# Kernel tuning notes

Measured on AMD Instinct MI355X. Metric: run time of the kernel, lower is better.

Reference implementation:

```python
import jax, jax.numpy as jnp
import numpy as np

N, F, E, C = 50000, 128, 800000, 10

def setup_inputs() -> dict:
    key = jax.random.key(0)
    ks = jax.random.split(key, 16)
    s = 1.0 / np.sqrt(F)
    def u(k, shape):
        return jax.random.uniform(k, shape, jnp.float32, -s, s)
    inp = {
        "x": jax.random.normal(ks[0], (N, F), jnp.float32),
        "edge_index": jax.random.randint(ks[1], (2, E), 0, N),
    }
    for i, p in enumerate(["1", "2"]):
        b = 2 + i * 5
        inp["W" + p] = u(ks[b], (F, F))          # EvolveGCNO initial_weight
        inp["wih" + p] = u(ks[b + 1], (3 * F, F))  # GRU input weights (r,z,n)
        inp["whh" + p] = u(ks[b + 2], (3 * F, F))  # GRU hidden weights
        inp["bih" + p] = u(ks[b + 3], (3 * F,))
        inp["bhh" + p] = u(ks[b + 4], (3 * F,))
    inp["lin_w"] = u(ks[12], (C, F))
    inp["lin_b"] = u(ks[13], (C,))
    return inp

def gru_step(x, h, wih, whh, bih, bhh):
    # torch.nn.GRU single step; gate order r, z, n
    gi = x @ wih.T + bih
    gh = h @ whh.T + bhh
    ir, iz, inn = jnp.split(gi, 3, axis=-1)
    hr, hz, hn = jnp.split(gh, 3, axis=-1)
    r = jax.nn.sigmoid(ir + hr)
    z = jax.nn.sigmoid(iz + hz)
    n = jnp.tanh(inn + r * hn)
    return (1.0 - z) * n + z * h

def gcn_conv(W, x, src, dst):
    # GCNConv_Fixed_W: gcn_norm with self-loops, then aggregate (x @ W)
    n = x.shape[0]
    loop = jnp.arange(n)
    s = jnp.concatenate([src, loop])
    d = jnp.concatenate([dst, loop])
    deg = jax.ops.segment_sum(jnp.ones(s.shape[0], x.dtype), d, num_segments=n)
    dinv = jnp.where(deg > 0, jax.lax.rsqrt(deg), 0.0)
    norm = dinv[s] * dinv[d]                 # [E+N]
    xw = x @ W                               # [N, F]
    return jax.ops.segment_sum(norm[:, None] * xw[s], d, num_segments=n)

def evolve_gcno(x, src, dst, W0, wih, whh, bih, bhh):
    # weight evolved by GRU with input = hidden = current weight
    W = gru_step(W0, W0, wih, whh, bih, bhh)
    return gcn_conv(W, x, src, dst)

def reference(x, edge_index, W1, wih1, whh1, bih1, bhh1,
              W2, wih2, whh2, bih2, bhh2, lin_w, lin_b):
    src, dst = edge_index[0], edge_index[1]
    h = jax.nn.relu(evolve_gcno(x, src, dst, W1, wih1, whh1, bih1, bhh1))
    # dropout is identity in eval mode
    h = jax.nn.relu(evolve_gcno(h, src, dst, W2, wih2, whh2, bih2, bhh2))
    logits = h @ lin_w.T + lin_b
    return jax.nn.log_softmax(logits, axis=1)
```

## Files before the change

kernel.cpp:

```cpp
#include <hip/hip_runtime.h>
#include <cstddef>
#include <cstdint>

#define F 128
#define C_OUT 10
#define SB 256

typedef short bf16x8 __attribute__((ext_vector_type(8)));
typedef float f32x4  __attribute__((ext_vector_type(4)));
typedef float f32x2  __attribute__((ext_vector_type(2)));

__device__ __forceinline__ unsigned short bf16_rne(float f) {
  unsigned u = __float_as_uint(f);
  return (unsigned short)((u + 0x7FFFu + ((u >> 16) & 1u)) >> 16);
}

__global__ void gru_evolve2_k(const float* __restrict__ W01, const float* __restrict__ wih1,
                              const float* __restrict__ whh1, const float* __restrict__ bih1,
                              const float* __restrict__ bhh1,
                              const float* __restrict__ W02, const float* __restrict__ wih2,
                              const float* __restrict__ whh2, const float* __restrict__ bih2,
                              const float* __restrict__ bhh2,
                              unsigned short* __restrict__ Bhi1, unsigned short* __restrict__ Bhi2,
                              int* __restrict__ counts, int n) {
  if ((int)blockIdx.x >= 128) {
    int i = ((int)blockIdx.x - 128) * SB + threadIdx.x;
    if (i < n) counts[i] = 0;
    return;
  }
  int t = blockIdx.x * 256 + threadIdx.x;
  int layer = t >> 14;
  int tt = t & 16383;
  const float* W0  = layer ? W02  : W01;
  const float* wih = layer ? wih2 : wih1;
  const float* whh = layer ? whh2 : whh1;
  const float* bih = layer ? bih2 : bih1;
  const float* bhh = layer ? bhh2 : bhh1;
  unsigned short* Bhi = layer ? Bhi2 : Bhi1;
  int i = tt >> 7, j = tt & 127;
  const float4* w0r = (const float4*)(W0 + (size_t)i * F);
  float gi[3], gh[3];
#pragma unroll
  for (int g = 0; g < 3; ++g) {
    const float4* wr = (const float4*)(wih + (size_t)(g * F + j) * F);
    const float4* hr = (const float4*)(whh + (size_t)(g * F + j) * F);
    float si = 0.f, sh = 0.f;
    for (int k = 0; k < F / 4; ++k) {
      float4 a = w0r[k];
      float4 b = wr[k];
      float4 c = hr[k];
      si += a.x * b.x + a.y * b.y + a.z * b.z + a.w * b.w;
      sh += a.x * c.x + a.y * c.y + a.z * c.z + a.w * c.w;
    }
    gi[g] = si + bih[g * F + j];
    gh[g] = sh + bhh[g * F + j];
  }
  float r = 1.0f / (1.0f + expf(-(gi[0] + gh[0])));
  float z = 1.0f / (1.0f + expf(-(gi[1] + gh[1])));
  float nn = tanhf(gi[2] + r * gh[2]);
  float val = (1.0f - z) * nn + z * W0[(size_t)i * F + j];

  int kstep = i >> 5, kl = i & 31;
  int lane = (kl >> 3) * 16 + (j & 15);
  int tile = j >> 4;
  int idx = ((kstep * 8 + tile) * 64 + lane) * 8 + (kl & 7);
  Bhi[idx] = bf16_rne(val);
}

__global__ void count_rank_k(const int* __restrict__ dst, int* __restrict__ counts,
                             int* __restrict__ rank, int E) {
  int e = blockIdx.x * blockDim.x + threadIdx.x;
  if (e < E) rank[e] = atomicAdd(&counts[dst[e]], 1);
}

__global__ void scan_local_k(const int* __restrict__ counts, int* __restrict__ incl,
                             int* __restrict__ blocksum, int n) {
  __shared__ int sh[SB];
  int gid = blockIdx.x * SB + threadIdx.x;
  int v = (gid < n) ? counts[gid] : 0;
  sh[threadIdx.x] = v;
  __syncthreads();
  for (int off = 1; off < SB; off <<= 1) {
    int t = 0;
    if ((int)threadIdx.x >= off) t = sh[threadIdx.x - off];
    __syncthreads();
    if ((int)threadIdx.x >= off) sh[threadIdx.x] += t;
    __syncthreads();
  }
  if (gid < n) incl[gid] = sh[threadIdx.x];
  if (threadIdx.x == SB - 1) blocksum[blockIdx.x] = sh[SB - 1];
}

__global__ void scan_finish_k(const int* __restrict__ counts, const int* __restrict__ incl,
                              const int* __restrict__ blocksum, int* __restrict__ rowptr,
                              float* __restrict__ dinv, int n, int nb) {
  __shared__ int sh[SB];
  __shared__ int orig[SB];
  int v = ((int)threadIdx.x < nb) ? blocksum[threadIdx.x] : 0;
  sh[threadIdx.x] = v;
  orig[threadIdx.x] = v;
  __syncthreads();
  for (int off = 1; off < SB; off <<= 1) {
    int t = 0;
    if ((int)threadIdx.x >= off) t = sh[threadIdx.x - off];
    __syncthreads();
    if ((int)threadIdx.x >= off) sh[threadIdx.x] += t;
    __syncthreads();
  }
  int myoff = sh[blockIdx.x] - orig[blockIdx.x];
  int gid = blockIdx.x * SB + threadIdx.x;
  if (gid >= n) return;
  int c = counts[gid];
  int inc = myoff + incl[gid];
  rowptr[gid] = inc - c;
  dinv[gid] = rsqrtf((float)c + 1.0f);
  if (gid == n - 1) rowptr[n] = inc;
}

__device__ __forceinline__ void fill_body(int bid, const int* __restrict__ src,
                                          const int* __restrict__ dst,
                                          const int* __restrict__ rank,
                                          const int* __restrict__ rowptr,
                                          int* __restrict__ csr_src, int E) {
  int e = bid * 256 + (int)threadIdx.x;
  if (e < E) {
    int d = dst[e];
    csr_src[rowptr[d] + rank[e]] = src[e] << 7;
  }
}

__device__ __forceinline__ void gemm_body(int bid, const float* __restrict__ X,
                                          const unsigned short* __restrict__ Bhi,
                                          const float* __restrict__ dinv,
                                          unsigned* __restrict__ Y, int nrows) {
  int wid = bid * 4 + ((int)threadIdx.x >> 6);
  int lane = threadIdx.x & 63;
  int ng = (nrows + 15) >> 4;
  if (wid >= ng) return;
  int g = __builtin_amdgcn_readfirstlane(wid);
  int q = lane >> 4, m = lane & 15;
  int rowA = g * 16 + m;
  if (rowA >= nrows) rowA = nrows - 1;

  f32x4 acc[8];
#pragma unroll
  for (int t = 0; t < 8; ++t) { acc[t].x = 0.f; acc[t].y = 0.f; acc[t].z = 0.f; acc[t].w = 0.f; }

#pragma unroll
  for (int s = 0; s < 4; ++s) {
    const float* xp = X + (size_t)rowA * F + s * 32 + q * 8;
    float4 xa = *(const float4*)xp;
    float4 xb = *(const float4*)(xp + 4);
    float xv[8] = {xa.x, xa.y, xa.z, xa.w, xb.x, xb.y, xb.z, xb.w};
    bf16x8 xh;
#pragma unroll
    for (int j = 0; j < 8; ++j) xh[j] = (short)bf16_rne(xv[j]);
#pragma unroll
    for (int t = 0; t < 8; ++t) {
      size_t boff = ((size_t)(s * 8 + t) * 64 + lane) * 8;
      bf16x8 wh = *(const bf16x8*)(Bhi + boff);
      acc[t] = __builtin_amdgcn_mfma_f32_16x16x32_bf16(wh, xh, acc[t], 0, 0, 0);
    }
  }

  int row = g * 16 + m;
  if (row < nrows) {
    float dd = dinv[row];
    unsigned* yr = Y + (size_t)row * 32 + q;
#pragma unroll
    for (int t = 0; t < 8; ++t) {
      int p = __builtin_amdgcn_cvt_pk_fp8_f32(dd * acc[t].x, dd * acc[t].y, 0, false);
      p = __builtin_amdgcn_cvt_pk_fp8_f32(dd * acc[t].z, dd * acc[t].w, p, true);
      yr[t * 4] = (unsigned)p;
    }
  }
}

__global__ void gemm_mfma_k(const float* __restrict__ X, const unsigned short* __restrict__ Bhi,
                            const float* __restrict__ dinv, unsigned* __restrict__ Y,
                            int nrows) {
  gemm_body(blockIdx.x, X, Bhi, dinv, Y, nrows);
}

__global__ void fill_gemm_k(const float* __restrict__ X, const unsigned short* __restrict__ Bhi,
                            const float* __restrict__ dinv, unsigned* __restrict__ Y,
                            int nrows, int ngemm,
                            const int* __restrict__ src, const int* __restrict__ dst,
                            const int* __restrict__ rank, const int* __restrict__ rowptr,
                            int* __restrict__ csr_src, int E) {
  if ((int)blockIdx.x < ngemm)
    gemm_body(blockIdx.x, X, Bhi, dinv, Y, nrows);
  else
    fill_body((int)blockIdx.x - ngemm, src, dst, rank, rowptr, csr_src, E);
}

template <bool FUSE_LOGITS>
__global__ void agg_fp8_k(const int* __restrict__ rowptr, const int* __restrict__ csr_src,
                          const float* __restrict__ dinv, const unsigned* __restrict__ xwp,
                          float* __restrict__ hout,
                          const float* __restrict__ lw, const float* __restrict__ lb,
                          float* __restrict__ outp, int n) {
  int wave = (int)((blockIdx.x * blockDim.x + threadIdx.x) >> 6);
  int lane = threadIdx.x & 63;
  if (wave >= n) return;
  int node = __builtin_amdgcn_readfirstlane(wave);
  int half = lane >> 5, hm = lane & 31;
  float dd = dinv[node];
  const char* __restrict__ cb = (const char*)xwp;
  unsigned loff = (unsigned)(hm << 2);
  f32x2 acc0 = {0.f, 0.f}, acc1 = {0.f, 0.f};
  f32x2 bcc0 = {0.f, 0.f}, bcc1 = {0.f, 0.f};

#define DEC(U, A, B)                                           \
  do {                                                         \
    (A) += __builtin_amdgcn_cvt_pk_f32_fp8((int)(U), false);   \
    (B) += __builtin_amdgcn_cvt_pk_f32_fp8((int)(U), true);    \
  } while (0)

  {
    unsigned u = *(const unsigned*)(cb + ((((unsigned)node) << 7) | loff));
    if (half) u = 0u;
    DEC(u, acc0, acc1);
  }

  int b = rowptr[node], e = rowptr[node + 1];
  int i = b;
  for (; i + 16 <= e; i += 16) {
    int s0 = csr_src[i + 0],  s1 = csr_src[i + 1],  s2 = csr_src[i + 2],  s3 = csr_src[i + 3];
    int s4 = csr_src[i + 4],  s5 = csr_src[i + 5],  s6 = csr_src[i + 6],  s7 = csr_src[i + 7];
    int s8 = csr_src[i + 8],  s9 = csr_src[i + 9],  sA = csr_src[i + 10], sB = csr_src[i + 11];
    int sC = csr_src[i + 12], sD = csr_src[i + 13], sE = csr_src[i + 14], sF = csr_src[i + 15];
    unsigned o0 = ((unsigned)(half ? s1 : s0)) | loff;
    unsigned o1 = ((unsigned)(half ? s3 : s2)) | loff;
    unsigned o2 = ((unsigned)(half ? s5 : s4)) | loff;
    unsigned o3 = ((unsigned)(half ? s7 : s6)) | loff;
    unsigned o4 = ((unsigned)(half ? s9 : s8)) | loff;
    unsigned o5 = ((unsigned)(half ? sB : sA)) | loff;
    unsigned o6 = ((unsigned)(half ? sD : sC)) | loff;
    unsigned o7 = ((unsigned)(half ? sF : sE)) | loff;
    unsigned u0 = *(const unsigned*)(cb + o0);
    unsigned u1 = *(const unsigned*)(cb + o1);
    unsigned u2 = *(const unsigned*)(cb + o2);
    unsigned u3 = *(const unsigned*)(cb + o3);
    unsigned u4 = *(const unsigned*)(cb + o4);
    unsigned u5 = *(const unsigned*)(cb + o5);
    unsigned u6 = *(const unsigned*)(cb + o6);
    unsigned u7 = *(const unsigned*)(cb + o7);
    DEC(u0, acc0, acc1);
    DEC(u1, bcc0, bcc1);
    DEC(u2, acc0, acc1);
    DEC(u3, bcc0, bcc1);
    DEC(u4, acc0, acc1);
    DEC(u5, bcc0, bcc1);
    DEC(u6, acc0, acc1);
    DEC(u7, bcc0, bcc1);
  }
  for (; i + 8 <= e; i += 8) {
    int s0 = csr_src[i + 0], s1 = csr_src[i + 1], s2 = csr_src[i + 2], s3 = csr_src[i + 3];
    int s4 = csr_src[i + 4], s5 = csr_src[i + 5], s6 = csr_src[i + 6], s7 = csr_src[i + 7];
    unsigned o0 = ((unsigned)(half ? s1 : s0)) | loff;
    unsigned o1 = ((unsigned)(half ? s3 : s2)) | loff;
    unsigned o2 = ((unsigned)(half ? s5 : s4)) | loff;
    unsigned o3 = ((unsigned)(half ? s7 : s6)) | loff;
    unsigned u0 = *(const unsigned*)(cb + o0);
    unsigned u1 = *(const unsigned*)(cb + o1);
    unsigned u2 = *(const unsigned*)(cb + o2);
    unsigned u3 = *(const unsigned*)(cb + o3);
    DEC(u0, acc0, acc1);
    DEC(u1, bcc0, bcc1);
    DEC(u2, acc0, acc1);
    DEC(u3, bcc0, bcc1);
  }
  for (; i + 2 <= e; i += 2) {
    int s0 = csr_src[i], s1 = csr_src[i + 1];
    unsigned o = ((unsigned)(half ? s1 : s0)) | loff;
    unsigned u = *(const unsigned*)(cb + o);
    DEC(u, acc0, acc1);
  }
  if (i < e) {
    int s = csr_src[i];
    unsigned u = *(const unsigned*)(cb + (((unsigned)s) | loff));
    if (half) u = 0u;
    DEC(u, acc0, acc1);
  }
#undef DEC
  acc0 += bcc0;
  acc1 += bcc1;

  acc0.x += __shfl_xor(acc0.x, 32);
  acc0.y += __shfl_xor(acc0.y, 32);
  acc1.x += __shfl_xor(acc1.x, 32);
  acc1.y += __shfl_xor(acc1.y, 32);

  float h0 = fmaxf(dd * acc0.x, 0.f);
  float h1 = fmaxf(dd * acc0.y, 0.f);
  float h2 = fmaxf(dd * acc1.x, 0.f);
  float h3 = fmaxf(dd * acc1.y, 0.f);

  if (!FUSE_LOGITS) {
    if (half == 0) {
      *(float4*)(hout + (size_t)node * F + hm * 4) = make_float4(h0, h1, h2, h3);
    }
  } else {
    float acc[C_OUT];
#pragma unroll
    for (int c = 0; c < C_OUT; ++c) {
      float4 w = *(const float4*)(lw + (size_t)c * F + hm * 4);
      float v = h0 * w.x + h1 * w.y + h2 * w.z + h3 * w.w;
      v += __shfl_xor(v, 1); v += __shfl_xor(v, 2);
      v += __shfl_xor(v, 4); v += __shfl_xor(v, 8);
      v += __shfl_xor(v, 16);
      acc[c] = v + lb[c];
    }
    float mx = acc[0];
#pragma unroll
    for (int c = 1; c < C_OUT; ++c) mx = fmaxf(mx, acc[c]);
    float s = 0.f;
#pragma unroll
    for (int c = 0; c < C_OUT; ++c) s += expf(acc[c] - mx);
    float lse = mx + logf(s);
#pragma unroll
    for (int c = 0; c < C_OUT; ++c)
      if (lane == c) outp[(size_t)node * C_OUT + c] = acc[c] - lse;
  }
}

extern "C" void kernel_launch(void* const* d_in, const int* in_sizes, int n_in,
                              void* d_out, int out_size, void* d_ws, size_t ws_size,
                              hipStream_t stream) {
  const float* x    = (const float*)d_in[0];
  const int*   ei   = (const int*)d_in[1];
  const float* W1   = (const float*)d_in[2];
  const float* wih1 = (const float*)d_in[3];
  const float* whh1 = (const float*)d_in[4];
  const float* bih1 = (const float*)d_in[5];
  const float* bhh1 = (const float*)d_in[6];
  const float* W2   = (const float*)d_in[7];
  const float* wih2 = (const float*)d_in[8];
  const float* whh2 = (const float*)d_in[9];
  const float* bih2 = (const float*)d_in[10];
  const float* bhh2 = (const float*)d_in[11];
  const float* lw   = (const float*)d_in[12];
  const float* lb   = (const float*)d_in[13];
  float* out = (float*)d_out;

  int N = in_sizes[0] / F;
  int E = in_sizes[1] / 2;
  const int* src = ei;
  const int* dst = ei + E;
  int nb = (N + SB - 1) / SB;
  int ng = (N + 15) / 16;
  int ngemm = (ng + 3) / 4;
  int nfill = (E + 255) / 256;
  int nagg = (N + 3) / 4;

  float* ws = (float*)d_ws;
  unsigned* bufA = (unsigned*)ws;
  float* bufB = (float*)(bufA + (size_t)N * 32);
  float* dinv = bufB + (size_t)N * F;
  unsigned short* Bhi1 = (unsigned short*)(dinv + N);
  unsigned short* Bhi2 = Bhi1 + F * F;
  int* counts = (int*)(Bhi2 + F * F);
  int* rowptr = counts + N;
  int* rank   = rowptr + N + 1;
  int* incl   = rank + E;
  int* blocksum = incl + N;
  int* csr_src = blocksum + 256;

  gru_evolve2_k<<<128 + nb, 256, 0, stream>>>(W1, wih1, whh1, bih1, bhh1,
                                              W2, wih2, whh2, bih2, bhh2,
                                              Bhi1, Bhi2, counts, N);

  count_rank_k<<<(E + 255) / 256, 256, 0, stream>>>(dst, counts, rank, E);
  scan_local_k<<<nb, SB, 0, stream>>>(counts, incl, blocksum, N);
  scan_finish_k<<<nb, SB, 0, stream>>>(counts, incl, blocksum, rowptr, dinv, N, nb);

  fill_gemm_k<<<ngemm + nfill, 256, 0, stream>>>(x, Bhi1, dinv, bufA, N, ngemm,
                                                 src, dst, rank, rowptr, csr_src, E);
  agg_fp8_k<false><<<nagg, 256, 0, stream>>>(rowptr, csr_src, dinv, bufA, bufB,
                                             nullptr, nullptr, nullptr, N);

  gemm_mfma_k<<<ngemm, 256, 0, stream>>>(bufB, Bhi2, dinv, bufA, N);
  agg_fp8_k<true><<<nagg, 256, 0, stream>>>(rowptr, csr_src, dinv, bufA, nullptr,
                                            lw, lb, out, N);
}
```

Measured before the change: 257.9 us.

## Gather 8 edges per wave with 16-byte fp8 row loads in aggregation

Reworks the sparse aggregation kernel so each wave splits into 8 groups of 8 lanes, each group gathering a whole fp8 row of a different neighbor with 16-byte vector loads, instead of two halves doing 4-byte loads. This cuts the number of load instructions per edge and raises edges in flight per wave. The cost is more accumulator registers and a three-step cross-group shuffle reduction. The fused logits/log-softmax epilogue is also redistributed across the new lane layout.

```diff
diff --git a/kernel.cpp b/kernel.cpp
--- a/kernel.cpp
+++ b/kernel.cpp
@@ -9,6 +9,7 @@
 typedef short bf16x8 __attribute__((ext_vector_type(8)));
 typedef float f32x4  __attribute__((ext_vector_type(4)));
 typedef float f32x2  __attribute__((ext_vector_type(2)));
+typedef unsigned u32x4 __attribute__((ext_vector_type(4)));
 
 __device__ __forceinline__ unsigned short bf16_rne(float f) {
   unsigned u = __float_as_uint(f);
@@ -204,124 +205,136 @@
   int lane = threadIdx.x & 63;
   if (wave >= n) return;
   int node = __builtin_amdgcn_readfirstlane(wave);
-  int half = lane >> 5, hm = lane & 31;
+  int g = lane >> 3, j = lane & 7;
+  unsigned j16 = (unsigned)(j << 4);
   float dd = dinv[node];
   const char* __restrict__ cb = (const char*)xwp;
-  unsigned loff = (unsigned)(hm << 2);
-  f32x2 acc0 = {0.f, 0.f}, acc1 = {0.f, 0.f};
-  f32x2 bcc0 = {0.f, 0.f}, bcc1 = {0.f, 0.f};
-
-#define DEC(U, A, B)                                           \
-  do {                                                         \
-    (A) += __builtin_amdgcn_cvt_pk_f32_fp8((int)(U), false);   \
-    (B) += __builtin_amdgcn_cvt_pk_f32_fp8((int)(U), true);    \
+
+  f32x2 acc[8], bcc[8];
+#pragma unroll
+  for (int k = 0; k < 8; ++k) {
+    acc[k].x = 0.f; acc[k].y = 0.f;
+    bcc[k].x = 0.f; bcc[k].y = 0.f;
+  }
+
+#define DEC4(U, A)                                                   \
+  do {                                                               \
+    A[0] += __builtin_amdgcn_cvt_pk_f32_fp8((int)(U)[0], false);     \
+    A[1] += __builtin_amdgcn_cvt_pk_f32_fp8((int)(U)[0], true);      \
+    A[2] += __builtin_amdgcn_cvt_pk_f32_fp8((int)(U)[1], false);     \
+    A[3] += __builtin_amdgcn_cvt_pk_f32_fp8((int)(U)[1], true);      \
+    A[4] += __builtin_amdgcn_cvt_pk_f32_fp8((int)(U)[2], false);     \
+    A[5] += __builtin_amdgcn_cvt_pk_f32_fp8((int)(U)[2], true);      \
+    A[6] += __builtin_amdgcn_cvt_pk_f32_fp8((int)(U)[3], false);     \
+    A[7] += __builtin_amdgcn_cvt_pk_f32_fp8((int)(U)[3], true);      \
   } while (0)
 
   {
-    unsigned u = *(const unsigned*)(cb + ((((unsigned)node) << 7) | loff));
-    if (half) u = 0u;
-    DEC(u, acc0, acc1);
+    u32x4 u = *(const u32x4*)(cb + ((((unsigned)node) << 7) | j16));
+    if (g) { u[0] = 0u; u[1] = 0u; u[2] = 0u; u[3] = 0u; }
+    DEC4(u, bcc);
   }
 
   int b = rowptr[node], e = rowptr[node + 1];
   int i = b;
+  for (; i + 32 <= e; i += 32) {
+    int t0 = csr_src[i + g];
+    int t1 = csr_src[i + 8 + g];
+    int t2 = csr_src[i + 16 + g];
+    int t3 = csr_src[i + 24 + g];
+    u32x4 u0 = *(const u32x4*)(cb + (((unsigned)t0) | j16));
+    u32x4 u1 = *(const u32x4*)(cb + (((unsigned)t1) | j16));
+    u32x4 u2 = *(const u32x4*)(cb + (((unsigned)t2) | j16));
+    u32x4 u3 = *(const u32x4*)(cb + (((unsigned)t3) | j16));
+    DEC4(u0, acc);
+    DEC4(u1, bcc);
+    DEC4(u2, acc);
+    DEC4(u3, bcc);
+  }
   for (; i + 16 <= e; i += 16) {
-    int s0 = csr_src[i + 0],  s1 = csr_src[i + 1],  s2 = csr_src[i + 2],  s3 = csr_src[i + 3];
-    int s4 = csr_src[i + 4],  s5 = csr_src[i + 5],  s6 = csr_src[i + 6],  s7 = csr_src[i + 7];
-    int s8 = csr_src[i + 8],  s9 = csr_src[i + 9],  sA = csr_src[i + 10], sB = csr_src[i + 11];
-    int sC = csr_src[i + 12], sD = csr_src[i + 13], sE = csr_src[i + 14], sF = csr_src[i + 15];
-    unsigned o0 = ((unsigned)(half ? s1 : s0)) | loff;
-    unsigned o1 = ((unsigned)(half ? s3 : s2)) | loff;
-    unsigned o2 = ((unsigned)(half ? s5 : s4)) | loff;
-    unsigned o3 = ((unsigned)(half ? s7 : s6)) | loff;
-    unsigned o4 = ((unsigned)(half ? s9 : s8)) | loff;
-    unsigned o5 = ((unsigned)(half ? sB : sA)) | loff;
-    unsigned o6 = ((unsigned)(half ? sD : sC)) | loff;
-    unsigned o7 = ((unsigned)(half ? sF : sE)) | loff;
-    unsigned u0 = *(const unsigned*)(cb + o0);
-    unsigned u1 = *(const unsigned*)(cb + o1);
-    unsigned u2 = *(const unsigned*)(cb + o2);
-    unsigned u3 = *(const unsigned*)(cb + o3);
-    unsigned u4 = *(const unsigned*)(cb + o4);
-    unsigned u5 = *(const unsigned*)(cb + o5);
-    unsigned u6 = *(const unsigned*)(cb + o6);
-    unsigned u7 = *(const unsigned*)(cb + o7);
-    DEC(u0, acc0, acc1);
-    DEC(u1, bcc0, bcc1);
-    DEC(u2, acc0, acc1);
-    DEC(u3, bcc0, bcc1);
-    DEC(u4, acc0, acc1);
-    DEC(u5, bcc0, bcc1);
-    DEC(u6, acc0, acc1);
-    DEC(u7, bcc0, bcc1);
-  }
-  for (; i + 8 <= e; i += 8) {
-    int s0 = csr_src[i + 0], s1 = csr_src[i + 1], s2 = csr_src[i + 2], s3 = csr_src[i + 3];
-    int s4 = csr_src[i + 4], s5 = csr_src[i + 5], s6 = csr_src[i + 6], s7 = csr_src[i + 7];
-    unsigned o0 = ((unsigned)(half ? s1 : s0)) | loff;
-    unsigned o1 = ((unsigned)(half ? s3 : s2)) | loff;
-    unsigned o2 = ((unsigned)(half ? s5 : s4)) | loff;
-    unsigned o3 = ((unsigned)(half ? s7 : s6)) | loff;
-    unsigned u0 = *(const unsigned*)(cb + o0);
-    unsigned u1 = *(const unsigned*)(cb + o1);
-    unsigned u2 = *(const unsigned*)(cb + o2);
-    unsigned u3 = *(const unsigned*)(cb + o3);
-    DEC(u0, acc0, acc1);
-    DEC(u1, bcc0, bcc1);
-    DEC(u2, acc0, acc1);
-    DEC(u3, bcc0, bcc1);
-  }
-  for (; i + 2 <= e; i += 2) {
-    int s0 = csr_src[i], s1 = csr_src[i + 1];
-    unsigned o = ((unsigned)(half ? s1 : s0)) | loff;
-    unsigned u = *(const unsigned*)(cb + o);
-    DEC(u, acc0, acc1);
+    int t0 = csr_src[i + g];
+    int t1 = csr_src[i + 8 + g];
+    u32x4 u0 = *(const u32x4*)(cb + (((unsigned)t0) | j16));
+    u32x4 u1 = *(const u32x4*)(cb + (((unsigned)t1) | j16));
+    DEC4(u0, acc);
+    DEC4(u1, bcc);
+  }
+  if (i + 8 <= e) {
+    int t0 = csr_src[i + g];
+    u32x4 u0 = *(const u32x4*)(cb + (((unsigned)t0) | j16));
+    DEC4(u0, acc);
+    i += 8;
   }
   if (i < e) {
-    int s = csr_src[i];
-    unsigned u = *(const unsigned*)(cb + (((unsigned)s) | loff));
-    if (half) u = 0u;
-    DEC(u, acc0, acc1);
-  }
-#undef DEC
-  acc0 += bcc0;
-  acc1 += bcc1;
-
-  acc0.x += __shfl_xor(acc0.x, 32);
-  acc0.y += __shfl_xor(acc0.y, 32);
-  acc1.x += __shfl_xor(acc1.x, 32);
-  acc1.y += __shfl_xor(acc1.y, 32);
-
-  float h0 = fmaxf(dd * acc0.x, 0.f);
-  float h1 = fmaxf(dd * acc0.y, 0.f);
-  float h2 = fmaxf(dd * acc1.x, 0.f);
-  float h3 = fmaxf(dd * acc1.y, 0.f);
+    int t = csr_src[i + g];
+    bool valid = (i + g) < e;
+    unsigned addr = valid ? (((unsigned)t) | j16) : j16;
+    u32x4 u = *(const u32x4*)(cb + addr);
+    if (!valid) { u[0] = 0u; u[1] = 0u; u[2] = 0u; u[3] = 0u; }
+    DEC4(u, bcc);
+  }
+#undef DEC4
+
+#pragma unroll
+  for (int k = 0; k < 8; ++k) { acc[k].x += bcc[k].x; acc[k].y += bcc[k].y; }
+
+#pragma unroll
+  for (int k = 0; k < 8; ++k) {
+    acc[k].x += __shfl_xor(acc[k].x, 8);
+    acc[k].y += __shfl_xor(acc[k].y, 8);
+    acc[k].x += __shfl_xor(acc[k].x, 16);
+    acc[k].y += __shfl_xor(acc[k].y, 16);
+    acc[k].x += __shfl_xor(acc[k].x, 32);
+    acc[k].y += __shfl_xor(acc[k].y, 32);
+  }
+
+  float hv[16];
+#pragma unroll
+  for (int k = 0; k < 8; ++k) {
+    hv[2 * k]     = fmaxf(dd * acc[k].x, 0.f);
+    hv[2 * k + 1] = fmaxf(dd * acc[k].y, 0.f);
+  }
 
   if (!FUSE_LOGITS) {
-    if (half == 0) {
-      *(float4*)(hout + (size_t)node * F + hm * 4) = make_float4(h0, h1, h2, h3);
+    if (g == 0) {
+      float4* hp = (float4*)(hout + (size_t)node * F + j * 16);
+      hp[0] = make_float4(hv[0], hv[1], hv[2], hv[3]);
+      hp[1] = make_float4(hv[4], hv[5], hv[6], hv[7]);
+      hp[2] = make_float4(hv[8], hv[9], hv[10], hv[11]);
+      hp[3] = make_float4(hv[12], hv[13], hv[14], hv[15]);
     }
   } else {
-    float acc[C_OUT];
-#pragma unroll
-    for (int c = 0; c < C_OUT; ++c) {
-      float4 w = *(const float4*)(lw + (size_t)c * F + hm * 4);
-      float v = h0 * w.x + h1 * w.y + h2 * w.z + h3 * w.w;
-      v += __shfl_xor(v, 1); v += __shfl_xor(v, 2);
-      v += __shfl_xor(v, 4); v += __shfl_xor(v, 8);
-      v += __shfl_xor(v, 16);
-      acc[c] = v + lb[c];
-    }
-    float mx = acc[0];
-#pragma unroll
-    for (int c = 1; c < C_OUT; ++c) mx = fmaxf(mx, acc[c]);
-    float s = 0.f;
-#pragma unroll
-    for (int c = 0; c < C_OUT; ++c) s += expf(acc[c] - mx);
-    float lse = mx + logf(s);
-#pragma unroll
-    for (int c = 0; c < C_OUT; ++c)
-      if (lane == c) outp[(size_t)node * C_OUT + c] = acc[c] - lse;
+    const float* w1 = lw + (size_t)g * F + j * 16;
+    float v1 = 0.f;
+#pragma unroll
+    for (int q = 0; q < 4; ++q) {
+      float4 w = *(const float4*)(w1 + q * 4);
+      v1 += hv[4 * q] * w.x + hv[4 * q + 1] * w.y + hv[4 * q + 2] * w.z + hv[4 * q + 3] * w.w;
+    }
+    float v2 = 0.f;
+    if (g < 2) {
+      const float* w2 = lw + (size_t)(8 + g) * F + j * 16;
+#pragma unroll
+      for (int q = 0; q < 4; ++q) {
+        float4 w = *(const float4*)(w2 + q * 4);
+        v2 += hv[4 * q] * w.x + hv[4 * q + 1] * w.y + hv[4 * q + 2] * w.z + hv[4 * q + 3] * w.w;
+      }
+    }
+    v1 += __shfl_xor(v1, 1); v1 += __shfl_xor(v1, 2); v1 += __shfl_xor(v1, 4);
+    v2 += __shfl_xor(v2, 1); v2 += __shfl_xor(v2, 2); v2 += __shfl_xor(v2, 4);
+    v1 += lb[g];
+    if (g < 2) v2 += lb[8 + g];
+    float m = (g < 2) ? fmaxf(v1, v2) : v1;
+    m = fmaxf(m, __shfl_xor(m, 8));
+    m = fmaxf(m, __shfl_xor(m, 16));
+    m = fmaxf(m, __shfl_xor(m, 32));
+    float ex = expf(v1 - m) + ((g < 2) ? expf(v2 - m) : 0.f);
+    ex += __shfl_xor(ex, 8); ex += __shfl_xor(ex, 16); ex += __shfl_xor(ex, 32);
+    float lse = m + logf(ex);
+    if (j == 0) {
+      outp[(size_t)node * C_OUT + g] = v1 - lse;
+      if (g < 2) outp[(size_t)node * C_OUT + 8 + g] = v2 - lse;
+    }
   }
 }
 
```

After: 293.4 us. 1.14x slower.
